# Performance work log

Hardware: AMD Instinct MI355X
Metric: run time of the kernel (lower is better)

Reference implementation:

```python
import jax, jax.numpy as jnp
import numpy as np

N_PEP = 50000
N_PROT = 50000
H = 256
F_IN = 1280
E = 300000
EL = 200000


def setup_inputs() -> dict:
    key = jax.random.key(0)
    ks = jax.random.split(key, 16)
    s = 0.02
    return {
        "x_pep": jax.random.normal(ks[0], (N_PEP, F_IN), jnp.float32),
        "x_prot": jax.random.normal(ks[1], (N_PROT, F_IN), jnp.float32),
        "Wpep": s * jax.random.normal(ks[2], (H, F_IN), jnp.float32),
        "bpep": jnp.zeros((H,), jnp.float32),
        "Wprot": s * jax.random.normal(ks[3], (H, F_IN), jnp.float32),
        "bprot": jnp.zeros((H,), jnp.float32),
        "Wl1": s * jax.random.normal(ks[4], (3, H, H), jnp.float32),
        "bl1": jnp.zeros((3, H), jnp.float32),
        "Wr1": s * jax.random.normal(ks[5], (3, H, H), jnp.float32),
        "Wl2": s * jax.random.normal(ks[6], (3, H, H), jnp.float32),
        "bl2": jnp.zeros((3, H), jnp.float32),
        "Wr2": s * jax.random.normal(ks[7], (3, H, H), jnp.float32),
        "ei_pp": jax.random.randint(ks[8], (2, E), 0, N_PEP, jnp.int32),   # pep -> prot
        "ei_rp": jax.random.randint(ks[9], (2, E), 0, N_PROT, jnp.int32),  # prot -> pep (reverse)
        "ei_prot": jax.random.randint(ks[10], (2, E), 0, N_PROT, jnp.int32),  # prot -> prot
        "eli_het": jax.random.randint(ks[11], (2, EL), 0, N_PEP, jnp.int32),
        "eli_homo": jax.random.randint(ks[12], (2, EL), 0, N_PROT, jnp.int32),
    }


def _seg_mean(src_feat, dst_idx, n_dst):
    # mean aggregation of edge messages into destination nodes
    s = jax.ops.segment_sum(src_feat, dst_idx, num_segments=n_dst)
    cnt = jax.ops.segment_sum(jnp.ones((dst_idx.shape[0], 1), src_feat.dtype), dst_idx, num_segments=n_dst)
    return s / jnp.maximum(cnt, 1.0)


def _sage(x_src, x_dst, ei, Wl, bl, Wr):
    # PyG SAGEConv(aggr='mean'): lin_l(mean_j x_j) + lin_r(x_i); lin_r has no bias
    m = _seg_mean(x_src[ei[0]], ei[1], x_dst.shape[0])
    return m @ Wl.T + bl + x_dst @ Wr.T


def reference(x_pep, x_prot, Wpep, bpep, Wprot, bprot,
              Wl1, bl1, Wr1, Wl2, bl2, Wr2,
              ei_pp, ei_rp, ei_prot, eli_het, eli_homo):
    # feat_src == 'esm': linear projection of ESM features
    h_pep = x_pep @ Wpep.T + bpep
    h_prot = x_prot @ Wprot.T + bprot

    # --- hetero SAGE layer 1 (to_hetero: sum over edge types per dst type) ---
    p1 = jax.nn.relu(_sage(h_prot, h_pep, ei_rp, Wl1[1], bl1[1], Wr1[1]))
    q1 = jax.nn.relu(_sage(h_pep, h_prot, ei_pp, Wl1[0], bl1[0], Wr1[0])
                     + _sage(h_prot, h_prot, ei_prot, Wl1[2], bl1[2], Wr1[2]))

    # --- hetero SAGE layer 2 ---
    p2 = _sage(q1, p1, ei_rp, Wl2[1], bl2[1], Wr2[1])
    q2 = (_sage(p1, q1, ei_pp, Wl2[0], bl2[0], Wr2[0])
          + _sage(q1, q1, ei_prot, Wl2[2], bl2[2], Wr2[2]))

    # edge classifiers: gather + elementwise mul + sum
    het_pred = (p2[eli_het[0]] * q2[eli_het[1]]).sum(axis=-1)
    homo_pred = (q2[eli_homo[0]] * q2[eli_homo[1]]).sum(axis=-1)
    return (het_pred, homo_pred)
```

## Files before the change

### kernel.cpp

```cpp
#include <hip/hip_runtime.h>

using u16 = unsigned short;
using u32 = unsigned int;

#define H 256
#define NNODE 50000
#define CAP 32
#define BM 128
#define BN 128
#define BK 64

typedef __attribute__((ext_vector_type(8))) short bf16x8;
typedef __attribute__((ext_vector_type(4))) float f32x4;
typedef __attribute__((ext_vector_type(4))) unsigned int u32x4;

struct AChunks { const void* p[3]; };

__device__ __forceinline__ u16 f2b(float f) {
    u32 u = __builtin_bit_cast(u32, f);
    return (u16)((u + 0x7FFFu + ((u >> 16) & 1u)) >> 16);
}
__device__ __forceinline__ float b2f(u16 h) {
    u32 u = ((u32)h) << 16;
    return __builtin_bit_cast(float, u);
}
__device__ __forceinline__ void gld_lds16(const void* g, void* l) {
    __builtin_amdgcn_global_load_lds(
        (__attribute__((address_space(1))) void*)(void*)g,
        (__attribute__((address_space(3))) void*)l, 16, 0, 0);
}
__device__ __forceinline__ u32 packbf(float a, float b) {
    return (u32)f2b(a) | ((u32)f2b(b) << 16);
}
__device__ __forceinline__ u32 pack_trunc(float lo, float hi) {
    return __builtin_amdgcn_perm(__builtin_bit_cast(u32, hi),
                                 __builtin_bit_cast(u32, lo), 0x07060302u);
}

template<bool RELU>
__global__ __launch_bounds__(512) void gemm_pipe(
    AChunks ac, int aStride, const u16* __restrict__ Bw,
    const float* __restrict__ bias, u16* __restrict__ C, int M, int Ktot)
{
    __shared__ __align__(16) char As[2][BM * 128];
    __shared__ __align__(16) char Bs[2][BN * 128];

    const int tid = threadIdx.x;
    const int l   = tid & 63;
    const int w   = tid >> 6;
    const int wr  = w >> 2, wc = w & 3;
    const int m0  = blockIdx.x * BM;
    const int n0  = blockIdx.y * BN;
    const int nk  = Ktot >> 6;

    f32x4 acc[4][2];
#pragma unroll
    for (int i = 0; i < 4; ++i)
#pragma unroll
        for (int j = 0; j < 2; ++j) acc[i][j] = f32x4{0.f, 0.f, 0.f, 0.f};

    auto stageB = [&](int k, int bi) {
        int k0 = k * 64;
#pragma unroll
        for (int i = 0; i < 2; ++i) {
            int ci = i * 512 + tid;
            int r = ci >> 3, c16 = ci & 7;
            int sb = (c16 * 16) ^ ((r & 7) << 4);
            const u16* g = Bw + (size_t)(n0 + r) * Ktot + k0 + (sb >> 1);
            gld_lds16(g, &Bs[bi][ci * 16]);
        }
    };
    auto stageAb = [&](int k, int bi) {
        int k0 = k * 64;
        const u16* base = (const u16*)ac.p[k0 >> 8];
        int kk = k0 & 255;
#pragma unroll
        for (int i = 0; i < 2; ++i) {
            int ci = i * 512 + tid;
            int r = ci >> 3, c16 = ci & 7;
            int row = m0 + r; row = row < M ? row : M - 1;
            int sb = (c16 * 16) ^ ((r & 7) << 4);
            const u16* g = base + (size_t)row * aStride + kk + (sb >> 1);
            gld_lds16(g, &As[bi][ci * 16]);
        }
    };
    auto compute = [&](int bi) {
#pragma unroll
        for (int ks = 0; ks < 2; ++ks) {
            bf16x8 af[4], bfr[2];
#pragma unroll
            for (int mi = 0; mi < 4; ++mi) {
                int r = wr * 64 + mi * 16 + (l & 15);
                int off = (ks * 64 + (l >> 4) * 16) ^ ((r & 7) << 4);
                af[mi] = *(const bf16x8*)&As[bi][r * 128 + off];
            }
#pragma unroll
            for (int ni = 0; ni < 2; ++ni) {
                int r = wc * 32 + ni * 16 + (l & 15);
                int off = (ks * 64 + (l >> 4) * 16) ^ ((r & 7) << 4);
                bfr[ni] = *(const bf16x8*)&Bs[bi][r * 128 + off];
            }
#pragma unroll
            for (int mi = 0; mi < 4; ++mi)
#pragma unroll
                for (int ni = 0; ni < 2; ++ni)
                    acc[mi][ni] = __builtin_amdgcn_mfma_f32_16x16x32_bf16(
                        af[mi], bfr[ni], acc[mi][ni], 0, 0, 0);
        }
    };
    auto body = [&](int k, int cur) {
        asm volatile("s_waitcnt vmcnt(4)" ::: "memory");
        __builtin_amdgcn_sched_barrier(0);
        __builtin_amdgcn_s_barrier();
        __builtin_amdgcn_sched_barrier(0);
        compute(cur);
        __builtin_amdgcn_sched_barrier(0);
        __builtin_amdgcn_s_barrier();
        __builtin_amdgcn_sched_barrier(0);
        int kq = k + 2; if (kq > nk - 1) kq = nk - 1;
        stageB(kq, cur);
        stageAb(kq, cur);
        __builtin_amdgcn_sched_barrier(0);
    };

    stageB(0, 0); stageAb(0, 0);
    __builtin_amdgcn_sched_barrier(0);
    stageB(1, 1); stageAb(1, 1);
    __builtin_amdgcn_sched_barrier(0);
    for (int k = 0; k < nk; k += 2) {
        body(k,     0);
        body(k + 1, 1);
    }

    const int fr = l & 15, fq = l >> 4;
#pragma unroll
    for (int ni = 0; ni < 2; ++ni) {
        int col = n0 + wc * 32 + ni * 16 + fr;
        float bv = bias ? bias[col] : 0.f;
#pragma unroll
        for (int mi = 0; mi < 4; ++mi) {
            int rowb = m0 + wr * 64 + mi * 16 + fq * 4;
#pragma unroll
            for (int j = 0; j < 4; ++j) {
                int row = rowb + j;
                if (row < M) {
                    float v = acc[mi][ni][j] + bv;
                    if (RELU) v = fmaxf(v, 0.f);
                    C[(size_t)row * H + col] = f2b(v);
                }
            }
        }
    }
}

__global__ __launch_bounds__(512) void gemm_proj(
    const float* __restrict__ A, int aStride, const u16* __restrict__ Bw,
    const float* __restrict__ bias, u16* __restrict__ C, int M, int Ktot)
{
    __shared__ __align__(16) char As[2][128 * 128];
    __shared__ __align__(16) char Bs[2][256 * 64];

    const int tid = threadIdx.x;
    const int l   = tid & 63;
    const int w   = tid >> 6;
    const int wr  = w >> 2, wc = w & 3;
    const int m0  = blockIdx.x * 128;
    const int nk  = Ktot >> 5;

    f32x4 acc[4][4];
#pragma unroll
    for (int i = 0; i < 4; ++i)
#pragma unroll
        for (int j = 0; j < 4; ++j) acc[i][j] = f32x4{0.f, 0.f, 0.f, 0.f};

    auto stageB = [&](int k, int bi) {
        int k0 = k * 32;
#pragma unroll
        for (int i = 0; i < 2; ++i) {
            int ci = i * 512 + tid;
            int r = ci >> 2, c4 = ci & 3;
            int sb = (c4 * 16) ^ ((r & 3) << 4);
            const u16* g = Bw + (size_t)r * Ktot + k0 + (sb >> 1);
            gld_lds16(g, &Bs[bi][ci * 16]);
        }
    };
    auto stageA = [&](int k, int bi) {
        int k0 = k * 32;
#pragma unroll
        for (int i = 0; i < 2; ++i) {
            int ci = i * 512 + tid;
            int r = ci >> 3, c8 = ci & 7;
            int row = m0 + r; row = row < M ? row : M - 1;
            int sb = (c8 * 16) ^ ((r & 7) << 4);
            const float* g = A + (size_t)row * aStride + k0 + (sb >> 2);
            gld_lds16(g, &As[bi][ci * 16]);
        }
    };
    auto compute = [&](int bi) {
        bf16x8 af[4], bfr[4];
#pragma unroll
        for (int mi = 0; mi < 4; ++mi) {
            int r = wr * 64 + mi * 16 + (l & 15);
            int o0 = ((l >> 4) * 32)      ^ ((r & 7) << 4);
            int o1 = ((l >> 4) * 32 + 16) ^ ((r & 7) << 4);
            f32x4 c0 = *(const f32x4*)&As[bi][r * 128 + o0];
            f32x4 c1 = *(const f32x4*)&As[bi][r * 128 + o1];
            u32x4 ww;
            ww[0] = pack_trunc(c0[0], c0[1]);
            ww[1] = pack_trunc(c0[2], c0[3]);
            ww[2] = pack_trunc(c1[0], c1[1]);
            ww[3] = pack_trunc(c1[2], c1[3]);
            af[mi] = __builtin_bit_cast(bf16x8, ww);
        }
#pragma unroll
        for (int ni = 0; ni < 4; ++ni) {
            int r = wc * 64 + ni * 16 + (l & 15);
            int off = ((l >> 4) * 16) ^ ((r & 3) << 4);
            bfr[ni] = *(const bf16x8*)&Bs[bi][r * 64 + off];
        }
#pragma unroll
        for (int mi = 0; mi < 4; ++mi)
#pragma unroll
            for (int ni = 0; ni < 4; ++ni)
                acc[mi][ni] = __builtin_amdgcn_mfma_f32_16x16x32_bf16(
                    af[mi], bfr[ni], acc[mi][ni], 0, 0, 0);
    };
    auto body = [&](int k, int cur) {
        asm volatile("s_waitcnt vmcnt(4)" ::: "memory");
        __builtin_amdgcn_sched_barrier(0);
        __builtin_amdgcn_s_barrier();
        __builtin_amdgcn_sched_barrier(0);
        compute(cur);
        __builtin_amdgcn_sched_barrier(0);
        __builtin_amdgcn_s_barrier();
        __builtin_amdgcn_sched_barrier(0);
        int kq = k + 2; if (kq > nk - 1) kq = nk - 1;
        stageB(kq, cur);
        stageA(kq, cur);
        __builtin_amdgcn_sched_barrier(0);
    };

    stageB(0, 0); stageA(0, 0);
    __builtin_amdgcn_sched_barrier(0);
    stageB(1, 1); stageA(1, 1);
    __builtin_amdgcn_sched_barrier(0);
    for (int k = 0; k < nk; k += 2) {
        body(k,     0);
        body(k + 1, 1);
    }

    const int fr = l & 15, fq = l >> 4;
#pragma unroll
    for (int ni = 0; ni < 4; ++ni) {
        int col = wc * 64 + ni * 16 + fr;
        float bv = bias ? bias[col] : 0.f;
#pragma unroll
        for (int mi = 0; mi < 4; ++mi) {
            int rowb = m0 + wr * 64 + mi * 16 + fq * 4;
#pragma unroll
            for (int j = 0; j < 4; ++j) {
                int row = rowb + j;
                if (row < M)
                    C[(size_t)row * H + col] = f2b(acc[mi][ni][j] + bv);
            }
        }
    }
}

__global__ __launch_bounds__(256) void fill_zero(float4* __restrict__ p, size_t n4)
{
    size_t i = (size_t)blockIdx.x * blockDim.x + threadIdx.x;
    size_t stride = (size_t)gridDim.x * blockDim.x;
    for (; i < n4; i += stride) p[i] = make_float4(0.f, 0.f, 0.f, 0.f);
}

__global__ __launch_bounds__(256) void build_bucket(
    const int* __restrict__ src, const int* __restrict__ dst, int nE,
    int* __restrict__ cnt, int* __restrict__ bucket)
{
    int i = blockIdx.x * blockDim.x + threadIdx.x;
    if (i >= nE) return;
    int d = dst[i];
    int pos = atomicAdd(&cnt[d], 1);
    if (pos < CAP) bucket[(size_t)d * CAP + pos] = src[i];
}

__global__ __launch_bounds__(256) void seg_mean_gather(
    const u16* __restrict__ feat, const int* __restrict__ bucket,
    const int* __restrict__ cnt, int n_dst, u16* __restrict__ out)
{
    int d = (int)(((size_t)blockIdx.x * blockDim.x + threadIdx.x) >> 6);
    int lane = threadIdx.x & 63;
    if (d >= n_dst) return;
    int c = cnt[d];
    int cc = c < CAP ? c : CAP;
    const int* b = bucket + (size_t)d * CAP;
    float a0 = 0.f, a1 = 0.f, a2 = 0.f, a3 = 0.f;
    int i = 0;
    for (; i + 4 <= cc; i += 4) {
        int s0 = b[i], s1 = b[i + 1], s2 = b[i + 2], s3 = b[i + 3];
        uint2 v0 = *(const uint2*)(feat + (size_t)s0 * H + lane * 4);
        uint2 v1 = *(const uint2*)(feat + (size_t)s1 * H + lane * 4);
        uint2 v2 = *(const uint2*)(feat + (size_t)s2 * H + lane * 4);
        uint2 v3 = *(const uint2*)(feat + (size_t)s3 * H + lane * 4);
        a0 += b2f((u16)(v0.x & 0xffff)) + b2f((u16)(v1.x & 0xffff))
            + b2f((u16)(v2.x & 0xffff)) + b2f((u16)(v3.x & 0xffff));
        a1 += b2f((u16)(v0.x >> 16)) + b2f((u16)(v1.x >> 16))
            + b2f((u16)(v2.x >> 16)) + b2f((u16)(v3.x >> 16));
        a2 += b2f((u16)(v0.y & 0xffff)) + b2f((u16)(v1.y & 0xffff))
            + b2f((u16)(v2.y & 0xffff)) + b2f((u16)(v3.y & 0xffff));
        a3 += b2f((u16)(v0.y >> 16)) + b2f((u16)(v1.y >> 16))
            + b2f((u16)(v2.y >> 16)) + b2f((u16)(v3.y >> 16));
    }
    for (; i < cc; ++i) {
        uint2 v = *(const uint2*)(feat + (size_t)b[i] * H + lane * 4);
        a0 += b2f((u16)(v.x & 0xffff));
        a1 += b2f((u16)(v.x >> 16));
        a2 += b2f((u16)(v.y & 0xffff));
        a3 += b2f((u16)(v.y >> 16));
    }
    float inv = 1.0f / fmaxf((float)c, 1.0f);
    uint2 o;
    o.x = packbf(a0 * inv, a1 * inv);
    o.y = packbf(a2 * inv, a3 * inv);
    *(uint2*)(out + (size_t)d * H + lane * 4) = o;
}

__global__ __launch_bounds__(256) void edge_dot(
    const u16* __restrict__ P, const u16* __restrict__ Q,
    const int* __restrict__ ia, const int* __restrict__ ib,
    int nE, float* __restrict__ out)
{
    int gi = blockIdx.x * 256 + threadIdx.x;
    int e = gi >> 5, l32 = gi & 31;
    if (e >= nE) return;
    uint4 a = *(const uint4*)(P + (size_t)ia[e] * H + l32 * 8);
    uint4 b = *(const uint4*)(Q + (size_t)ib[e] * H + l32 * 8);
    float v = 0.f;
    v += b2f((u16)(a.x & 0xffff)) * b2f((u16)(b.x & 0xffff));
    v += b2f((u16)(a.x >> 16))    * b2f((u16)(b.x >> 16));
    v += b2f((u16)(a.y & 0xffff)) * b2f((u16)(b.y & 0xffff));
    v += b2f((u16)(a.y >> 16))    * b2f((u16)(b.y >> 16));
    v += b2f((u16)(a.z & 0xffff)) * b2f((u16)(b.z & 0xffff));
    v += b2f((u16)(a.z >> 16))    * b2f((u16)(b.z >> 16));
    v += b2f((u16)(a.w & 0xffff)) * b2f((u16)(b.w & 0xffff));
    v += b2f((u16)(a.w >> 16))    * b2f((u16)(b.w >> 16));
#pragma unroll
    for (int off = 16; off; off >>= 1) v += __shfl_xor(v, off);
    if (l32 == 0) out[e] = v;
}

struct PackTab {
    const float* s1[12]; const float* s2[12]; u16* dst[12];
    int Ks[12], Kdst[12], koff[12], blk0[13];
};
__global__ __launch_bounds__(256) void pack_all(PackTab t)
{
    int b = blockIdx.x;
    int it = 0;
    while (it < 11 && b >= t.blk0[it + 1]) ++it;
    int idx = (b - t.blk0[it]) * 1024 + threadIdx.x * 4;
    int Ks = t.Ks[it];
    if (idx >= 256 * Ks) return;
    int n = idx / Ks;
    int k = idx - n * Ks;
    float4 v = *(const float4*)(t.s1[it] + idx);
    if (t.s2[it]) {
        float4 u = *(const float4*)(t.s2[it] + idx);
        v.x += u.x; v.y += u.y; v.z += u.z; v.w += u.w;
    }
    ushort4 h;
    h.x = f2b(v.x); h.y = f2b(v.y); h.z = f2b(v.z); h.w = f2b(v.w);
    *(ushort4*)(t.dst[it] + (size_t)n * t.Kdst[it] + t.koff[it] + k) = h;
}

__global__ void bias_pair(const float* __restrict__ bl1, const float* __restrict__ bl2,
                          float* __restrict__ bq1, float* __restrict__ bq2)
{
    int i = threadIdx.x;
    if (blockIdx.x == 0) bq1[i] = bl1[i] + bl1[512 + i];
    else                 bq2[i] = bl2[i] + bl2[512 + i];
}

static inline void launch_gemm3(const void* a0, const void* a1, const void* a2,
                                const u16* Bw, const float* bias, u16* C,
                                int Ktot, bool relu, hipStream_t s)
{
    AChunks ac = {{a0, a1, a2}};
    dim3 grid((NNODE + BM - 1) / BM, H / BN);
    if (relu) gemm_pipe<true><<<grid, 512, 0, s>>>(ac, 256, Bw, bias, C, NNODE, Ktot);
    else      gemm_pipe<false><<<grid, 512, 0, s>>>(ac, 256, Bw, bias, C, NNODE, Ktot);
}

extern "C" void kernel_launch(void* const* d_in, const int* in_sizes, int n_in,
                              void* d_out, int out_size, void* d_ws, size_t ws_size,
                              hipStream_t stream)
{
    const float* x_pep  = (const float*)d_in[0];
    const float* x_prot = (const float*)d_in[1];
    const float* Wpep   = (const float*)d_in[2];
    const float* bpep   = (const float*)d_in[3];
    const float* Wprot  = (const float*)d_in[4];
    const float* bprot  = (const float*)d_in[5];
    const float* Wl1    = (const float*)d_in[6];
    const float* bl1    = (const float*)d_in[7];
    const float* Wr1    = (const float*)d_in[8];
    const float* Wl2    = (const float*)d_in[9];
    const float* bl2    = (const float*)d_in[10];
    const float* Wr2    = (const float*)d_in[11];
    const int* ei_pp    = (const int*)d_in[12];
    const int* ei_rp    = (const int*)d_in[13];
    const int* ei_prot  = (const int*)d_in[14];
    const int* eli_het  = (const int*)d_in[15];
    const int* eli_homo = (const int*)d_in[16];

    const int E  = in_sizes[12] / 2;
    const int EL = in_sizes[15] / 2;
    const int FIN = in_sizes[2] / H;

    float* out = (float*)d_out;

    const size_t nodeElems = (size_t)NNODE * H;
    u16* bufA = (u16*)d_ws;
    u16* bufB = bufA + nodeElems;
    u16* bufC = bufB + nodeElems;
    u16* bufD = bufC + nodeElems;
    u16* bufE = bufD + nodeElems;
    u16* bufF = bufE + nodeElems;
    u16* Bpep  = bufF + nodeElems;
    u16* Bprot = Bpep  + (size_t)256 * 1280;
    u16* Bp1   = Bprot + (size_t)256 * 1280;
    u16* Bq1   = Bp1   + (size_t)256 * 512;
    u16* Bp2   = Bq1   + (size_t)256 * 768;
    u16* Bq2   = Bp2   + (size_t)256 * 512;
    float* bq1 = (float*)(Bq2 + (size_t)256 * 768);
    float* bq2 = bq1 + 256;
    int* cntRP   = (int*)(bq2 + 256);
    int* cntPP   = cntRP + NNODE;
    int* cntPR   = cntPP + NNODE;
    int* bktRP   = cntPR + NNODE;
    int* bktPP   = bktRP + (size_t)NNODE * CAP;
    int* bktPR   = bktPP + (size_t)NNODE * CAP;

    const size_t HH = (size_t)H * H;

    PackTab t{};
    int blk = 0, it = 0;
    auto add = [&](const float* s1, const float* s2, u16* d, int Ks, int Kd, int ko) {
        t.s1[it] = s1; t.s2[it] = s2; t.dst[it] = d;
        t.Ks[it] = Ks; t.Kdst[it] = Kd; t.koff[it] = ko;
        t.blk0[it] = blk; blk += (256 * Ks) / 1024; ++it;
    };
    add(Wpep,  nullptr, Bpep,  1280, 1280, 0);
    add(Wprot, nullptr, Bprot, 1280, 1280, 0);
    add(Wl1 + 1 * HH, nullptr,      Bp1, 256, 512, 0);
    add(Wr1 + 1 * HH, nullptr,      Bp1, 256, 512, 256);
    add(Wl1 + 0 * HH, nullptr,      Bq1, 256, 768, 0);
    add(Wl1 + 2 * HH, nullptr,      Bq1, 256, 768, 256);
    add(Wr1 + 0 * HH, Wr1 + 2 * HH, Bq1, 256, 768, 512);
    add(Wl2 + 1 * HH, nullptr,      Bp2, 256, 512, 0);
    add(Wr2 + 1 * HH, nullptr,      Bp2, 256, 512, 256);
    add(Wl2 + 0 * HH, nullptr,      Bq2, 256, 768, 0);
    add(Wl2 + 2 * HH, nullptr,      Bq2, 256, 768, 256);
    add(Wr2 + 0 * HH, Wr2 + 2 * HH, Bq2, 256, 768, 512);
    t.blk0[12] = blk;
    pack_all<<<blk, 256, 0, stream>>>(t);
    bias_pair<<<2, 256, 0, stream>>>(bl1, bl2, bq1, bq2);

    fill_zero<<<147, 256, 0, stream>>>((float4*)cntRP, (size_t)3 * NNODE / 4);
    build_bucket<<<(E + 255) / 256, 256, 0, stream>>>(ei_rp,   ei_rp + E,   E, cntRP, bktRP);
    build_bucket<<<(E + 255) / 256, 256, 0, stream>>>(ei_pp,   ei_pp + E,   E, cntPP, bktPP);
    build_bucket<<<(E + 255) / 256, 256, 0, stream>>>(ei_prot, ei_prot + E, E, cntPR, bktPR);

    {
        dim3 grid((NNODE + 127) / 128, 1);
        gemm_proj<<<grid, 512, 0, stream>>>(x_pep,  FIN, Bpep,  bpep,  bufA, NNODE, FIN);
        gemm_proj<<<grid, 512, 0, stream>>>(x_prot, FIN, Bprot, bprot, bufB, NNODE, FIN);
    }

    const int gG = (NNODE * 64 + 255) / 256;
    seg_mean_gather<<<gG, 256, 0, stream>>>(bufB, bktRP, cntRP, NNODE, bufE);
    launch_gemm3(bufE, bufA, nullptr, Bp1, bl1 + 256, bufC, 512, true, stream);
    seg_mean_gather<<<gG, 256, 0, stream>>>(bufA, bktPP, cntPP, NNODE, bufE);
    seg_mean_gather<<<gG, 256, 0, stream>>>(bufB, bktPR, cntPR, NNODE, bufF);
    launch_gemm3(bufE, bufF, bufB, Bq1, bq1, bufD, 768, true, stream);

    seg_mean_gather<<<gG, 256, 0, stream>>>(bufD, bktRP, cntRP, NNODE, bufE);
    launch_gemm3(bufE, bufC, nullptr, Bp2, bl2 + 256, bufA, 512, false, stream);
    seg_mean_gather<<<gG, 256, 0, stream>>>(bufC, bktPP, cntPP, NNODE, bufE);
    seg_mean_gather<<<gG, 256, 0, stream>>>(bufD, bktPR, cntPR, NNODE, bufF);
    launch_gemm3(bufE, bufF, bufD, Bq2, bq2, bufB, 768, false, stream);

    edge_dot<<<(EL * 32 + 255) / 256, 256, 0, stream>>>(bufA, bufB, eli_het,  eli_het  + EL, EL, out);
    edge_dot<<<(EL * 32 + 255) / 256, 256, 0, stream>>>(bufB, bufB, eli_homo, eli_homo + EL, EL, out + EL);
}
```

Before: 660.2 us.

## Enlarge projection GEMM tile to 256 rows with triple-buffered LDS pipeline

The fp32-input projection GEMM now uses 1024-thread blocks covering 256 rows, which halves the number of times the weight tile is loaded per row. Its two-stage LDS double buffer becomes a three-stage ring that prefetches three k-steps ahead, aiming to hide more global-load latency on this memory-bound GEMM. The B-tile swizzle is changed to match the new loading pattern. The cost is roughly 144KB of LDS per block, so only one block fits per CU, and the grid has fewer blocks (196), which can leave CUs underused and gives less latency hiding across blocks.

Measured after the change: 637.0 us. 3.5% less time.

```diff
diff --git a/kernel.cpp b/kernel.cpp
--- a/kernel.cpp
+++ b/kernel.cpp
@@ -153,18 +153,18 @@
     }
 }
 
-__global__ __launch_bounds__(512) void gemm_proj(
+__global__ __launch_bounds__(1024) void gemm_proj(
     const float* __restrict__ A, int aStride, const u16* __restrict__ Bw,
     const float* __restrict__ bias, u16* __restrict__ C, int M, int Ktot)
 {
-    __shared__ __align__(16) char As[2][128 * 128];
-    __shared__ __align__(16) char Bs[2][256 * 64];
+    __shared__ __align__(16) char As[3][256 * 128];
+    __shared__ __align__(16) char Bs[3][256 * 64];
 
     const int tid = threadIdx.x;
     const int l   = tid & 63;
     const int w   = tid >> 6;
-    const int wr  = w >> 2, wc = w & 3;
-    const int m0  = blockIdx.x * 128;
+    const int wq  = w >> 2, wc = w & 3;
+    const int m0  = blockIdx.x * 256;
     const int nk  = Ktot >> 5;
 
     f32x4 acc[4][4];
@@ -173,38 +173,39 @@
 #pragma unroll
         for (int j = 0; j < 4; ++j) acc[i][j] = f32x4{0.f, 0.f, 0.f, 0.f};
 
-    auto stageB = [&](int k, int bi) {
+    auto stage = [&](int k, int bi) {
         int k0 = k * 32;
+        char* asb = &As[0][0] + bi * (256 * 128);
+        char* bsb = &Bs[0][0] + bi * (256 * 64);
+        {
+            int ci = tid;
+            int r = ci >> 2, c4 = ci & 3;
+            int sb = (c4 * 16) ^ (((r >> 2) & 3) << 4);
+            const u16* g = Bw + (size_t)r * Ktot + k0 + (sb >> 1);
+            gld_lds16(g, bsb + ci * 16);
+        }
 #pragma unroll
         for (int i = 0; i < 2; ++i) {
-            int ci = i * 512 + tid;
-            int r = ci >> 2, c4 = ci & 3;
-            int sb = (c4 * 16) ^ ((r & 3) << 4);
-            const u16* g = Bw + (size_t)r * Ktot + k0 + (sb >> 1);
-            gld_lds16(g, &Bs[bi][ci * 16]);
-        }
-    };
-    auto stageA = [&](int k, int bi) {
-        int k0 = k * 32;
-#pragma unroll
-        for (int i = 0; i < 2; ++i) {
-            int ci = i * 512 + tid;
+            int ci = i * 1024 + tid;
             int r = ci >> 3, c8 = ci & 7;
             int row = m0 + r; row = row < M ? row : M - 1;
             int sb = (c8 * 16) ^ ((r & 7) << 4);
             const float* g = A + (size_t)row * aStride + k0 + (sb >> 2);
-            gld_lds16(g, &As[bi][ci * 16]);
-        }
-    };
+            gld_lds16(g, asb + ci * 16);
+        }
+    };
+
     auto compute = [&](int bi) {
+        const char* asb = &As[0][0] + bi * (256 * 128);
+        const char* bsb = &Bs[0][0] + bi * (256 * 64);
         bf16x8 af[4], bfr[4];
 #pragma unroll
         for (int mi = 0; mi < 4; ++mi) {
-            int r = wr * 64 + mi * 16 + (l & 15);
-            int o0 = ((l >> 4) * 32)      ^ ((r & 7) << 4);
-            int o1 = ((l >> 4) * 32 + 16) ^ ((r & 7) << 4);
-            f32x4 c0 = *(const f32x4*)&As[bi][r * 128 + o0];
-            f32x4 c1 = *(const f32x4*)&As[bi][r * 128 + o1];
+            int r = wq * 64 + mi * 16 + (l & 15);
+            int sw = (r & 7) << 4;
+            int base = (l >> 4) * 32;
+            f32x4 c0 = *(const f32x4*)(asb + r * 128 + (base ^ sw));
+            f32x4 c1 = *(const f32x4*)(asb + r * 128 + ((base + 16) ^ sw));
             u32x4 ww;
             ww[0] = pack_trunc(c0[0], c0[1]);
             ww[1] = pack_trunc(c0[2], c0[3]);
@@ -215,8 +216,8 @@
 #pragma unroll
         for (int ni = 0; ni < 4; ++ni) {
             int r = wc * 64 + ni * 16 + (l & 15);
-            int off = ((l >> 4) * 16) ^ ((r & 3) << 4);
-            bfr[ni] = *(const bf16x8*)&Bs[bi][r * 64 + off];
+            int off = ((l >> 4) * 16) ^ (((r >> 2) & 3) << 4);
+            bfr[ni] = *(const bf16x8*)(bsb + r * 64 + off);
         }
 #pragma unroll
         for (int mi = 0; mi < 4; ++mi)
@@ -225,8 +226,14 @@
                 acc[mi][ni] = __builtin_amdgcn_mfma_f32_16x16x32_bf16(
                     af[mi], bfr[ni], acc[mi][ni], 0, 0, 0);
     };
-    auto body = [&](int k, int cur) {
-        asm volatile("s_waitcnt vmcnt(4)" ::: "memory");
+
+    stage(0, 0); __builtin_amdgcn_sched_barrier(0);
+    stage(1, 1); __builtin_amdgcn_sched_barrier(0);
+    stage(2, 2); __builtin_amdgcn_sched_barrier(0);
+
+    int cur = 0;
+    for (int k = 0; k < nk; ++k) {
+        asm volatile("s_waitcnt vmcnt(6)" ::: "memory");
         __builtin_amdgcn_sched_barrier(0);
         __builtin_amdgcn_s_barrier();
         __builtin_amdgcn_sched_barrier(0);
@@ -234,20 +241,12 @@
         __builtin_amdgcn_sched_barrier(0);
         __builtin_amdgcn_s_barrier();
         __builtin_amdgcn_sched_barrier(0);
-        int kq = k + 2; if (kq > nk - 1) kq = nk - 1;
-        stageB(kq, cur);
-        stageA(kq, cur);
-        __builtin_amdgcn_sched_barrier(0);
-    };
-
-    stageB(0, 0); stageA(0, 0);
-    __builtin_amdgcn_sched_barrier(0);
-    stageB(1, 1); stageA(1, 1);
-    __builtin_amdgcn_sched_barrier(0);
-    for (int k = 0; k < nk; k += 2) {
-        body(k,     0);
-        body(k + 1, 1);
-    }
+        int kq = k + 3; if (kq > nk - 1) kq = nk - 1;
+        stage(kq, cur);
+        __builtin_amdgcn_sched_barrier(0);
+        cur = (cur == 2) ? 0 : cur + 1;
+    }
+    asm volatile("s_waitcnt vmcnt(0)" ::: "memory");
 
     const int fr = l & 15, fq = l >> 4;
 #pragma unroll
@@ -256,7 +255,7 @@
         float bv = bias ? bias[col] : 0.f;
 #pragma unroll
         for (int mi = 0; mi < 4; ++mi) {
-            int rowb = m0 + wr * 64 + mi * 16 + fq * 4;
+            int rowb = m0 + wq * 64 + mi * 16 + fq * 4;
 #pragma unroll
             for (int j = 0; j < 4; ++j) {
                 int row = rowb + j;
@@ -473,9 +472,9 @@
     build_bucket<<<(E + 255) / 256, 256, 0, stream>>>(ei_prot, ei_prot + E, E, cntPR, bktPR);
 
     {
-        dim3 grid((NNODE + 127) / 128, 1);
-        gemm_proj<<<grid, 512, 0, stream>>>(x_pep,  FIN, Bpep,  bpep,  bufA, NNODE, FIN);
-        gemm_proj<<<grid, 512, 0, stream>>>(x_prot, FIN, Bprot, bprot, bufB, NNODE, FIN);
+        dim3 grid((NNODE + 255) / 256, 1);
+        gemm_proj<<<grid, 1024, 0, stream>>>(x_pep,  FIN, Bpep,  bpep,  bufA, NNODE, FIN);
+        gemm_proj<<<grid, 1024, 0, stream>>>(x_prot, FIN, Bprot, bprot, bufB, NNODE, FIN);
     }
 
     const int gG = (NNODE * 64 + 255) / 256;
```

## Pre-convert projection inputs to tiled bf16 before the projection GEMM

Applied to the files above, without the earlier changes.

Adds a conversion kernel that turns the fp32 ESM features into bf16 and stores them in a blocked layout of 32-row by 32-column tiles. The projection GEMM then loads bf16 A tiles directly into LDS, so it no longer converts fp32 to bf16 in the inner loop and its A staging halves. The trade is an extra full read of the fp32 inputs plus a bf16 write and re-read through a workspace buffer. Conversion also changes from truncation to round-to-nearest.

After: 722.1 us. +9.4%, slower.

```diff
diff --git a/kernel.cpp b/kernel.cpp
--- a/kernel.cpp
+++ b/kernel.cpp
@@ -9,10 +9,11 @@
 #define BM 128
 #define BN 128
 #define BK 64
+#define FINK 1280
+#define NB 1563
 
 typedef __attribute__((ext_vector_type(8))) short bf16x8;
 typedef __attribute__((ext_vector_type(4))) float f32x4;
-typedef __attribute__((ext_vector_type(4))) unsigned int u32x4;
 
 struct AChunks { const void* p[3]; };
 
@@ -31,10 +32,6 @@
 }
 __device__ __forceinline__ u32 packbf(float a, float b) {
     return (u32)f2b(a) | ((u32)f2b(b) << 16);
-}
-__device__ __forceinline__ u32 pack_trunc(float lo, float hi) {
-    return __builtin_amdgcn_perm(__builtin_bit_cast(u32, hi),
-                                 __builtin_bit_cast(u32, lo), 0x07060302u);
 }
 
 template<bool RELU>
@@ -70,7 +67,7 @@
             gld_lds16(g, &Bs[bi][ci * 16]);
         }
     };
-    auto stageAb = [&](int k, int bi) {
+    auto stageA = [&](int k, int bi) {
         int k0 = k * 64;
         const u16* base = (const u16*)ac.p[k0 >> 8];
         int kk = k0 & 255;
@@ -119,13 +116,13 @@
         __builtin_amdgcn_sched_barrier(0);
         int kq = k + 2; if (kq > nk - 1) kq = nk - 1;
         stageB(kq, cur);
-        stageAb(kq, cur);
-        __builtin_amdgcn_sched_barrier(0);
-    };
-
-    stageB(0, 0); stageAb(0, 0);
+        stageA(kq, cur);
+        __builtin_amdgcn_sched_barrier(0);
+    };
+
+    stageB(0, 0); stageA(0, 0);
     __builtin_amdgcn_sched_barrier(0);
-    stageB(1, 1); stageAb(1, 1);
+    stageB(1, 1); stageA(1, 1);
     __builtin_amdgcn_sched_barrier(0);
     for (int k = 0; k < nk; k += 2) {
         body(k,     0);
@@ -153,11 +150,11 @@
     }
 }
 
-__global__ __launch_bounds__(512) void gemm_proj(
-    const float* __restrict__ A, int aStride, const u16* __restrict__ Bw,
+__global__ __launch_bounds__(512) void gemm_proj32(
+    const u16* __restrict__ A, const u16* __restrict__ Bw,
     const float* __restrict__ bias, u16* __restrict__ C, int M, int Ktot)
 {
-    __shared__ __align__(16) char As[2][128 * 128];
+    __shared__ __align__(16) char As[2][128 * 64];
     __shared__ __align__(16) char Bs[2][256 * 64];
 
     const int tid = threadIdx.x;
@@ -173,6 +170,14 @@
 #pragma unroll
         for (int j = 0; j < 4; ++j) acc[i][j] = f32x4{0.f, 0.f, 0.f, 0.f};
 
+    auto stageA = [&](int k, int bi) {
+        int ci = tid;
+        int r = ci >> 2, c4 = ci & 3;
+        int R = m0 + r; R = R < M ? R : M - 1;
+        int sb = (c4 * 16) ^ ((r & 3) << 4);
+        const u16* g = A + ((size_t)k * NB + (R >> 5)) * 1024 + (R & 31) * 32 + (sb >> 1);
+        gld_lds16(g, &As[bi][ci * 16]);
+    };
     auto stageB = [&](int k, int bi) {
         int k0 = k * 32;
 #pragma unroll
@@ -184,33 +189,13 @@
             gld_lds16(g, &Bs[bi][ci * 16]);
         }
     };
-    auto stageA = [&](int k, int bi) {
-        int k0 = k * 32;
-#pragma unroll
-        for (int i = 0; i < 2; ++i) {
-            int ci = i * 512 + tid;
-            int r = ci >> 3, c8 = ci & 7;
-            int row = m0 + r; row = row < M ? row : M - 1;
-            int sb = (c8 * 16) ^ ((r & 7) << 4);
-            const float* g = A + (size_t)row * aStride + k0 + (sb >> 2);
-            gld_lds16(g, &As[bi][ci * 16]);
-        }
-    };
     auto compute = [&](int bi) {
         bf16x8 af[4], bfr[4];
 #pragma unroll
         for (int mi = 0; mi < 4; ++mi) {
             int r = wr * 64 + mi * 16 + (l & 15);
-            int o0 = ((l >> 4) * 32)      ^ ((r & 7) << 4);
-            int o1 = ((l >> 4) * 32 + 16) ^ ((r & 7) << 4);
-            f32x4 c0 = *(const f32x4*)&As[bi][r * 128 + o0];
-            f32x4 c1 = *(const f32x4*)&As[bi][r * 128 + o1];
-            u32x4 ww;
-            ww[0] = pack_trunc(c0[0], c0[1]);
-            ww[1] = pack_trunc(c0[2], c0[3]);
-            ww[2] = pack_trunc(c1[0], c1[1]);
-            ww[3] = pack_trunc(c1[2], c1[3]);
-            af[mi] = __builtin_bit_cast(bf16x8, ww);
+            int off = ((l >> 4) * 16) ^ ((r & 3) << 4);
+            af[mi] = *(const bf16x8*)&As[bi][r * 64 + off];
         }
 #pragma unroll
         for (int ni = 0; ni < 4; ++ni) {
@@ -226,7 +211,7 @@
                     af[mi], bfr[ni], acc[mi][ni], 0, 0, 0);
     };
     auto body = [&](int k, int cur) {
-        asm volatile("s_waitcnt vmcnt(4)" ::: "memory");
+        asm volatile("s_waitcnt vmcnt(3)" ::: "memory");
         __builtin_amdgcn_sched_barrier(0);
         __builtin_amdgcn_s_barrier();
         __builtin_amdgcn_sched_barrier(0);
@@ -248,12 +233,13 @@
         body(k,     0);
         body(k + 1, 1);
     }
+    asm volatile("s_waitcnt vmcnt(0)" ::: "memory");
 
     const int fr = l & 15, fq = l >> 4;
 #pragma unroll
     for (int ni = 0; ni < 4; ++ni) {
         int col = wc * 64 + ni * 16 + fr;
-        float bv = bias ? bias[col] : 0.f;
+        float bv = bias[col];
 #pragma unroll
         for (int mi = 0; mi < 4; ++mi) {
             int rowb = m0 + wr * 64 + mi * 16 + fq * 4;
@@ -264,6 +250,40 @@
                     C[(size_t)row * H + col] = f2b(acc[mi][ni][j] + bv);
             }
         }
+    }
+}
+
+__global__ __launch_bounds__(256) void cvt8(
+    const float* __restrict__ in, u16* __restrict__ outp, int M)
+{
+    __shared__ __align__(16) u16 lds[8][1288];
+    const int b = blockIdx.x;
+    const int r0 = b * 8;
+    const int tid = threadIdx.x;
+    const int rb  = r0 >> 5;
+    const int rr0 = r0 & 31;
+
+    const float* src = in + (size_t)r0 * FINK;
+#pragma unroll
+    for (int it = 0; it < 10; ++it) {
+        int c = it * 256 + tid;
+        int row = c / 320;
+        int col = (c - row * 320) * 4;
+        float4 v = *(const float4*)(src + row * FINK + col);
+        uint2 pr;
+        pr.x = packbf(v.x, v.y);
+        pr.y = packbf(v.z, v.w);
+        *(uint2*)&lds[row][col] = pr;
+    }
+    __syncthreads();
+
+    const int row = (tid >> 3) & 7, c8 = tid & 7;
+#pragma unroll
+    for (int it = 0; it < 10; ++it) {
+        int t = it * 4 + (tid >> 6);
+        uint2 v = *(const uint2*)&lds[row][t * 32 + c8 * 4];
+        u16* dst = outp + ((size_t)t * NB + rb) * 1024 + (rr0 + row) * 32 + c8 * 4;
+        *(uint2*)dst = v;
     }
 }
 
@@ -416,7 +436,6 @@
 
     const int E  = in_sizes[12] / 2;
     const int EL = in_sizes[15] / 2;
-    const int FIN = in_sizes[2] / H;
 
     float* out = (float*)d_out;
 
@@ -441,6 +460,8 @@
     int* bktRP   = cntPR + NNODE;
     int* bktPP   = bktRP + (size_t)NNODE * CAP;
     int* bktPR   = bktPP + (size_t)NNODE * CAP;
+    u16* xbPep   = (u16*)(bktPR + (size_t)NNODE * CAP);
+    u16* xbProt  = xbPep + (size_t)40 * NB * 1024;
 
     const size_t HH = (size_t)H * H;
 
@@ -474,8 +495,10 @@
 
     {
         dim3 grid((NNODE + 127) / 128, 1);
-        gemm_proj<<<grid, 512, 0, stream>>>(x_pep,  FIN, Bpep,  bpep,  bufA, NNODE, FIN);
-        gemm_proj<<<grid, 512, 0, stream>>>(x_prot, FIN, Bprot, bprot, bufB, NNODE, FIN);
+        cvt8<<<NNODE / 8, 256, 0, stream>>>(x_pep, xbPep, NNODE);
+        gemm_proj32<<<grid, 512, 0, stream>>>(xbPep, Bpep, bpep, bufA, NNODE, FINK);
+        cvt8<<<NNODE / 8, 256, 0, stream>>>(x_prot, xbProt, NNODE);
+        gemm_proj32<<<grid, 512, 0, stream>>>(xbProt, Bprot, bprot, bufB, NNODE, FINK);
     }
 
     const int gG = (NNODE * 64 + 255) / 256;
```
